# Performance work log

Measured on AMD Instinct MI355X. Metric: run time of the kernel, lower is better.

Reference implementation:

```python
import jax, jax.numpy as jnp
import numpy as np

DIM = 96
HEADS = 6
WS = 8                      # window_size
OWS = int(WS * 0.5) + WS    # overlap_win_size = 12
PAD = (OWS - WS) // 2       # 2
Dd = Hh = Ww = 24
B = 1
L = Dd * Hh * Ww
MLP_H = DIM * 2
TBL = (WS + OWS - 1) ** 3   # 6859 relative-position-bias entries


def setup_inputs() -> dict:
    key = jax.random.key(0)
    ks = jax.random.split(key, 8)
    def n(k, shape, s=0.02):
        return jax.random.normal(k, shape, jnp.float32) * s
    return {
        "x": jax.random.normal(ks[0], (B, L, DIM), jnp.float32),
        "ln1_w": jnp.ones((DIM,), jnp.float32),
        "ln1_b": jnp.zeros((DIM,), jnp.float32),
        "qkv_w": n(ks[1], (3 * DIM, DIM)),
        "qkv_b": jnp.zeros((3 * DIM,), jnp.float32),
        "rpb": n(ks[2], (TBL, HEADS)),
        "proj_w": n(ks[3], (DIM, DIM)),
        "proj_b": jnp.zeros((DIM,), jnp.float32),
        "ln2_w": jnp.ones((DIM,), jnp.float32),
        "ln2_b": jnp.zeros((DIM,), jnp.float32),
        "fc1_w": n(ks[4], (MLP_H, DIM)),
        "fc1_b": jnp.zeros((MLP_H,), jnp.float32),
        "fc2_w": n(ks[5], (DIM, MLP_H)),
        "fc2_b": jnp.zeros((DIM,), jnp.float32),
        "rpi": jax.random.randint(ks[6], (WS ** 3, OWS ** 3), 0, TBL),
        "D": Dd, "H": Hh, "W": Ww,
    }


def _ln(x, w, b):
    m = jnp.mean(x, -1, keepdims=True)
    v = jnp.var(x, -1, keepdims=True)
    return (x - m) / jnp.sqrt(v + 1e-5) * w + b


def _ocab3d(x, ln1_w, ln1_b, qkv_w, qkv_b, rpb, proj_w, proj_b,
            ln2_w, ln2_b, fc1_w, fc1_b, fc2_w, fc2_b, rpi, D, H, W):
    Bz, Lz, C = x.shape
    hd = C // HEADS
    scale = hd ** -0.5
    shortcut = x

    xn = _ln(x, ln1_w, ln1_b).reshape(Bz, D, H, W, C)
    qkv = xn @ qkv_w.T + qkv_b                   # [B,D,H,W,3C]
    q = qkv[..., :C]
    kv = qkv[..., C:]                            # cat(k, v) on channels, [B,D,H,W,2C]

    nD, nH, nW = D // WS, H // WS, W // WS
    nw = nD * nH * nW

    # non-overlapping query windows -> [B*nw, WS^3, C]
    qw = q.reshape(Bz, nD, WS, nH, WS, nW, WS, C)
    qw = qw.transpose(0, 1, 3, 5, 2, 4, 6, 7).reshape(Bz * nw, WS ** 3, C)

    # overlapping kv windows via pad + strided gather (mirrors F.pad + unfold)
    kvp = jnp.pad(kv, ((0, 0), (PAD, PAD), (PAD, PAD), (PAD, PAD), (0, 0)))
    idx_d = (jnp.arange(nD) * WS)[:, None] + jnp.arange(OWS)[None, :]
    idx_h = (jnp.arange(nH) * WS)[:, None] + jnp.arange(OWS)[None, :]
    idx_w = (jnp.arange(nW) * WS)[:, None] + jnp.arange(OWS)[None, :]
    kw = kvp[:, idx_d]                 # [B,nD,OWS,Hp,Wp,2C]
    kw = kw[:, :, :, idx_h]            # [B,nD,OWS,nH,OWS,Wp,2C]
    kw = kw[:, :, :, :, :, idx_w]      # [B,nD,OWS,nH,OWS,nW,OWS,2C]
    kw = kw.transpose(0, 1, 3, 5, 2, 4, 6, 7).reshape(Bz * nw, OWS ** 3, 2 * C)
    kk, vv = kw[..., :C], kw[..., C:]

    qh = qw.reshape(-1, WS ** 3, HEADS, hd).transpose(0, 2, 1, 3) * scale
    kh = kk.reshape(-1, OWS ** 3, HEADS, hd).transpose(0, 2, 1, 3)
    vh = vv.reshape(-1, OWS ** 3, HEADS, hd).transpose(0, 2, 1, 3)

    attn = jnp.einsum('bhqd,bhkd->bhqk', qh, kh)               # [B*nw,H,512,1728]
    bias = rpb[rpi.reshape(-1)].reshape(WS ** 3, OWS ** 3, HEADS).transpose(2, 0, 1)
    attn = jax.nn.softmax(attn + bias[None], axis=-1)
    out = jnp.einsum('bhqk,bhkd->bhqd', attn, vh)
    out = out.transpose(0, 2, 1, 3).reshape(Bz * nw, WS ** 3, C)

    # window reverse -> [B, L, C]
    out = out.reshape(Bz, nD, nH, nW, WS, WS, WS, C)
    out = out.transpose(0, 1, 4, 2, 5, 3, 6, 7).reshape(Bz, D * H * W, C)

    x2 = out @ proj_w.T + proj_b + shortcut
    h1 = jax.nn.gelu(_ln(x2, ln2_w, ln2_b) @ fc1_w.T + fc1_b, approximate=False)
    return x2 + (h1 @ fc2_w.T + fc2_b)


def reference(x, ln1_w, ln1_b, qkv_w, qkv_b, rpb, proj_w, proj_b,
              ln2_w, ln2_b, fc1_w, fc1_b, fc2_w, fc2_b, rpi, D, H, W):
    return _ocab3d(x, ln1_w, ln1_b, qkv_w, qkv_b, rpb, proj_w, proj_b,
                   ln2_w, ln2_b, fc1_w, fc1_b, fc2_w, fc2_b, rpi, D, H, W)
```

## Files before the change

### kernel.cpp

```cpp
#include <hip/hip_runtime.h>
#include <math.h>

#define DIMC   96
#define NHEADS 6
#define HD     16
#define WSZ    8
#define OWSZ   12
#define PADW   2
#define DD     24
#define LTOK   13824
#define NWIN   27
#define NKEY   1728
#define NROW   512
#define MLPH   192
#define PDIM   28
#define PD3    21952
#define TBL    6859
#define LSTR   82944
#define AOSTR  1327104

typedef __attribute__((ext_vector_type(4))) short bf16x4;
typedef __attribute__((ext_vector_type(8))) short bf16x8;
typedef __attribute__((ext_vector_type(4))) float f32x4;

__device__ __forceinline__ unsigned short bfround(float f) {
    unsigned u = __float_as_uint(f);
    return (unsigned short)((u + 0x7FFFu + ((u >> 16) & 1u)) >> 16);
}
__device__ __forceinline__ unsigned bfpack(float a, float b) {
    unsigned ua = __float_as_uint(a), ub = __float_as_uint(b);
    ua = (ua + 0x7FFFu + ((ua >> 16) & 1u)) >> 16;
    ub = (ub + 0x7FFFu + ((ub >> 16) & 1u)) >> 16;
    return ua | (ub << 16);
}
__device__ __forceinline__ uint4 pack8(const float* v) {
    uint4 u;
    u.x = bfpack(v[0], v[1]); u.y = bfpack(v[2], v[3]);
    u.z = bfpack(v[4], v[5]); u.w = bfpack(v[6], v[7]);
    return u;
}
__device__ __forceinline__ bf16x4 pack4(f32x4 p) {
    union { uint2 u; bf16x4 v; } r;
    r.u.x = __builtin_amdgcn_perm(__float_as_uint(p[1]), __float_as_uint(p[0]), 0x07060302u);
    r.u.y = __builtin_amdgcn_perm(__float_as_uint(p[3]), __float_as_uint(p[2]), 0x07060302u);
    return r.v;
}
__device__ __forceinline__ f32x4 mfma16(bf16x4 a, bf16x4 b, f32x4 c) {
#if __has_builtin(__builtin_amdgcn_mfma_f32_16x16x16bf16_1k)
    return __builtin_amdgcn_mfma_f32_16x16x16bf16_1k(a, b, c, 0, 0, 0);
#else
    bf16x8 a8 = {a[0], a[1], a[2], a[3], 0, 0, 0, 0};
    bf16x8 b8 = {b[0], b[1], b[2], b[3], 0, 0, 0, 0};
    return __builtin_amdgcn_mfma_f32_16x16x32_bf16(a8, b8, c, 0, 0, 0);
#endif
}

#define QKVB 1296
#define ZB   515
#define WPB  45
__global__ __launch_bounds__(256) void qkvz_kernel(
        const float* __restrict__ X, const float* __restrict__ W,
        const float* __restrict__ bias, const float* __restrict__ lnw,
        const float* __restrict__ lnb,
        const float* __restrict__ projw, const float* __restrict__ fc1w,
        const float* __restrict__ fc2w,
        unsigned short* __restrict__ q16, unsigned short* __restrict__ kvp2,
        uint4* __restrict__ wpack) {
    __shared__ uint4 Af4[2 * 3 * 4 * 16];
    __shared__ uint4 Bf4[6 * 3 * 4 * 16];
    int bx = blockIdx.x, tid = threadIdx.x;

    if (bx >= QKVB + ZB) {
        int u = (bx - QKVB - ZB) * 256 + tid;
        if (u < 5760) {
            int p = (u < 1152) ? u : (u < 3456 ? (u - 1152) % 1152 : (u - 3456) % 1152);
            int nn = p & 15, r = p >> 4, qg = r & 3, r2 = r >> 2;
            int kt = r2 % 3, ct = r2 / 3;
            int n = ct * 16 + nn, g = kt * 4 + qg;
            const float* src;
            if (u < 1152)      src = projw + n * 96 + g * 8;
            else if (u < 3456) { int nc = (u - 1152) / 1152; src = fc1w + (long)(nc * 96 + n) * 96 + g * 8; }
            else               { int kh = (u - 3456) / 1152; src = fc2w + (long)n * 192 + kh * 96 + g * 8; }
            const float4* s4 = (const float4*)src;
            float v[8];
            float4 t0 = s4[0], t1 = s4[1];
            v[0]=t0.x; v[1]=t0.y; v[2]=t0.z; v[3]=t0.w;
            v[4]=t1.x; v[5]=t1.y; v[6]=t1.z; v[7]=t1.w;
            wpack[u] = pack8(v);
        }
        return;
    }
    if (bx >= QKVB) {
        int t = (bx - QKVB) * 256 + tid;
        if (t < 21952 * 6) {
            int head = t / PD3, pos = t % PD3;
            int d = pos / 784, h = (pos / 28) % 28, w = pos % 28;
            if (d < 2 || d >= 26 || h < 2 || h >= 26 || w < 2 || w >= 26) {
                uint4* p = (uint4*)(kvp2 + ((long)head * PD3 + pos) * 32);
                uint4 z = make_uint4(0, 0, 0, 0);
                p[0] = z; p[1] = z; p[2] = z; p[3] = z;
            }
        }
        return;
    }

    int nc   = bx % 3;
    int row0 = (bx / 3) * 32;

    if (tid < 128) {
        int row = tid >> 2, part = tid & 3;
        int rt = row >> 4, mm = row & 15;
        float v[24];
        const float4* xp = (const float4*)(X + (long)(row0 + row) * 96 + part * 24);
        float s = 0.f, sq = 0.f;
        #pragma unroll
        for (int i = 0; i < 6; ++i) {
            float4 t = xp[i];
            v[i*4+0] = t.x; v[i*4+1] = t.y; v[i*4+2] = t.z; v[i*4+3] = t.w;
            s  += t.x + t.y + t.z + t.w;
            sq += t.x*t.x + t.y*t.y + t.z*t.z + t.w*t.w;
        }
        s  += __shfl_xor(s, 1);  s  += __shfl_xor(s, 2);
        sq += __shfl_xor(sq, 1); sq += __shfl_xor(sq, 2);
        float mean = s * (1.f / 96.f);
        float inv  = rsqrtf(sq * (1.f / 96.f) - mean * mean + 1e-5f);
        const float4* wp = (const float4*)(lnw + part * 24);
        const float4* bp = (const float4*)(lnb + part * 24);
        #pragma unroll
        for (int i = 0; i < 6; ++i) {
            float4 wv = wp[i], bv = bp[i];
            v[i*4+0] = (v[i*4+0] - mean) * inv * wv.x + bv.x;
            v[i*4+1] = (v[i*4+1] - mean) * inv * wv.y + bv.y;
            v[i*4+2] = (v[i*4+2] - mean) * inv * wv.z + bv.z;
            v[i*4+3] = (v[i*4+3] - mean) * inv * wv.w + bv.w;
        }
        #pragma unroll
        for (int gg = 0; gg < 3; ++gg) {
            int g = part * 3 + gg;
            int kt = g >> 2, qq = g & 3;
            Af4[((rt * 3 + kt) * 4 + qq) * 16 + mm] = pack8(v + gg * 8);
        }
    }
    for (int idx = tid; idx < 96 * 12; idx += 256) {
        int n = idx / 12;
        int g = idx % 12;
        const float4* wp = (const float4*)(W + (long)(nc * 96 + n) * 96 + g * 8);
        float v[8];
        float4 t0 = wp[0], t1 = wp[1];
        v[0]=t0.x; v[1]=t0.y; v[2]=t0.z; v[3]=t0.w;
        v[4]=t1.x; v[5]=t1.y; v[6]=t1.z; v[7]=t1.w;
        int ct = n >> 4, nn = n & 15, kt = g >> 2, qg = g & 3;
        Bf4[((ct * 3 + kt) * 4 + qg) * 16 + nn] = pack8(v);
    }
    __syncthreads();

    int wave = tid >> 6, lane = tid & 63;
    int qq = lane >> 4, mI = lane & 15;
    int rt = wave & 1, cg = wave >> 1;

    f32x4 acc[3];
    #pragma unroll
    for (int j = 0; j < 3; ++j) acc[j] = (f32x4){0.f, 0.f, 0.f, 0.f};
    #pragma unroll
    for (int kt = 0; kt < 3; ++kt) {
        bf16x8 a = *(const bf16x8*)&Af4[((rt * 3 + kt) * 4 + qq) * 16 + mI];
        #pragma unroll
        for (int j = 0; j < 3; ++j) {
            bf16x8 b = *(const bf16x8*)&Bf4[(((cg * 3 + j) * 3 + kt) * 4 + qq) * 16 + mI];
            acc[j] = __builtin_amdgcn_mfma_f32_16x16x32_bf16(a, b, acc[j], 0, 0, 0);
        }
    }

    float bv[3];
    #pragma unroll
    for (int j = 0; j < 3; ++j) bv[j] = bias[nc * 96 + (cg * 3 + j) * 16 + mI];
    #pragma unroll
    for (int r = 0; r < 4; ++r) {
        int row = row0 + rt * 16 + qq * 4 + r;
        if (nc == 0) {
            unsigned short* op = q16 + (long)row * 96;
            #pragma unroll
            for (int j = 0; j < 3; ++j)
                op[(cg * 3 + j) * 16 + mI] = bfround(0.25f * (acc[j][r] + bv[j]));
        } else {
            int d = row / 576, hh = (row / 24) % 24, w2 = row % 24;
            long pos = ((long)(d + 2) * 28 + (hh + 2)) * 28 + (w2 + 2);
            #pragma unroll
            for (int j = 0; j < 3; ++j) {
                int head = cg * 3 + j;
                kvp2[((long)head * PD3 + pos) * 32 +
                     (nc == 2 ? 16 : 0) + mI] = bfround(acc[j][r] + bv[j]);
            }
        }
    }
}

__global__ __launch_bounds__(256) void bias_kernel(
        const int* __restrict__ rpi, const float* __restrict__ rpb,
        float* __restrict__ biasP) {
    int bx = blockIdx.x;
    int head = bx / 216;
    int r2 = bx % 216;
    int kt = r2 >> 1, qh = r2 & 1;
    int k0 = kt * 16;
    int qi = qh * 256 + threadIdx.x;
    const int* rp = rpi + (long)qi * NKEY + k0;
    int idx[16];
    #pragma unroll
    for (int j = 0; j < 4; ++j) {
        int4 t = *(const int4*)(rp + j * 4);
        idx[j*4+0] = t.x; idx[j*4+1] = t.y; idx[j*4+2] = t.z; idx[j*4+3] = t.w;
    }
    #pragma unroll
    for (int quad = 0; quad < 4; ++quad) {
        float4 v;
        v.x = rpb[idx[quad*4+0] * NHEADS + head];
        v.y = rpb[idx[quad*4+1] * NHEADS + head];
        v.z = rpb[idx[quad*4+2] * NHEADS + head];
        v.w = rpb[idx[quad*4+3] * NHEADS + head];
        *(float4*)(biasP + ((((long)head*108 + kt)*4 + quad)*512 + qi)*4) = v;
    }
}

#define KSTR 20
#define VSTR 68
__global__ __launch_bounds__(256) void attn_kernel(
        const unsigned short* __restrict__ q, const unsigned short* __restrict__ kvp2,
        const float* __restrict__ biasP, float* __restrict__ ao,
        float* __restrict__ lbuf) {
    __shared__ unsigned short Ks[2][64 * KSTR];
    __shared__ unsigned short Vs[2][16 * VSTR];
    int bid = blockIdx.x;
    int w = bid / 48, rem = bid % 48;
    int head = rem >> 3;
    int quart = (rem >> 1) & 3, half = rem & 1;
    int wd8 = (w / 9) * 8, wh8 = ((w / 3) % 3) * 8, ww8 = (w % 3) * 8;
    int tid = threadIdx.x, wave = tid >> 6, lane = tid & 63;
    int quad = lane >> 4, m16 = lane & 15;
    int key = tid >> 2, part = tid & 3;
    int c0 = half ? 13 : 0;
    int cn = half ? 14 : 13;

    auto kvaddr = [&](int c) -> const uint4* {
        int jg = c * 64 + key;
        int i = jg / 144, jh = (jg / 12) % 12, jw = jg % 12;
        long sp = ((long)(wd8 + i) * PDIM + (wh8 + jh)) * PDIM + (ww8 + jw);
        return (const uint4*)(kvp2 + ((long)head * PD3 + sp) * 32 + part * 8);
    };
    auto writeLDS = [&](int b, uint4 v) {
        if (part < 2) {
            *(uint2*)(&Ks[b][key * KSTR + part * 8])     = make_uint2(v.x, v.y);
            *(uint2*)(&Ks[b][key * KSTR + part * 8 + 4]) = make_uint2(v.z, v.w);
        } else {
            int d0 = (part - 2) * 8;
            Vs[b][(d0+0)*VSTR + key] = (unsigned short)(v.x);
            Vs[b][(d0+1)*VSTR + key] = (unsigned short)(v.x >> 16);
            Vs[b][(d0+2)*VSTR + key] = (unsigned short)(v.y);
            Vs[b][(d0+3)*VSTR + key] = (unsigned short)(v.y >> 16);
            Vs[b][(d0+4)*VSTR + key] = (unsigned short)(v.z);
            Vs[b][(d0+5)*VSTR + key] = (unsigned short)(v.z >> 16);
            Vs[b][(d0+6)*VSTR + key] = (unsigned short)(v.w);
            Vs[b][(d0+7)*VSTR + key] = (unsigned short)(v.w >> 16);
        }
    };

    int grow[2]; bf16x4 qf[2];
    #pragma unroll
    for (int qt = 0; qt < 2; ++qt) {
        int ql = quart * 128 + wave * 32 + qt * 16 + m16;
        int ld = ql >> 6, lh = (ql >> 3) & 7, lw = ql & 7;
        grow[qt] = ((wd8 + ld) * 24 + (wh8 + lh)) * 24 + (ww8 + lw);
        qf[qt] = *(const bf16x4*)(q + (long)grow[qt] * 96 + head * 16 + quad * 4);
    }

    const float* bbase = biasP + (long)head * 884736 + quad * 2048
                         + ((quart * 128 + wave * 32 + m16) << 2);
    f32x4 bcur[2][4];
    #pragma unroll
    for (int qt = 0; qt < 2; ++qt)
        #pragma unroll
        for (int kt = 0; kt < 4; ++kt)
            bcur[qt][kt] = *(const f32x4*)(bbase + (long)(c0*4 + kt) * 8192 + qt * 64);

    writeLDS(0, *kvaddr(c0));

    f32x4 o[2];
    o[0] = (f32x4){0.f,0.f,0.f,0.f}; o[1] = (f32x4){0.f,0.f,0.f,0.f};
    float l[2] = {0.f, 0.f};
    uint4 stgn;

    #pragma unroll 1
    for (int cc = 0; cc < cn; ++cc) {
        int c = c0 + cc;
        if (cc + 1 < cn) stgn = *kvaddr(c + 1);
        __syncthreads();
        int b = cc & 1;

        bf16x4 kf[4];
        #pragma unroll
        for (int kt = 0; kt < 4; ++kt)
            kf[kt] = *(const bf16x4*)(&Ks[b][(kt * 16 + m16) * KSTR + quad * 4]);

        f32x4 S[2][4];
        #pragma unroll
        for (int qt = 0; qt < 2; ++qt)
            #pragma unroll
            for (int kt = 0; kt < 4; ++kt)
                S[qt][kt] = mfma16(kf[kt], qf[qt], bcur[qt][kt]);

        f32x4 bnxt[2][4];
        if (cc + 1 < cn) {
            const float* bp = bbase + (long)(c + 1) * 32768;
            #pragma unroll
            for (int qt = 0; qt < 2; ++qt)
                #pragma unroll
                for (int kt = 0; kt < 4; ++kt)
                    bnxt[qt][kt] = *(const f32x4*)(bp + kt * 8192 + qt * 64);
        }

        #pragma unroll
        for (int qt = 0; qt < 2; ++qt) {
            float ls = 0.f;
            #pragma unroll
            for (int kt = 0; kt < 4; ++kt)
                #pragma unroll
                for (int r = 0; r < 4; ++r) {
                    float p = __expf(S[qt][kt][r]);
                    S[qt][kt][r] = p; ls += p;
                }
            l[qt] += ls;
        }

        #pragma unroll
        for (int kt = 0; kt < 4; ++kt) {
            bf16x4 vf = *(const bf16x4*)(&Vs[b][m16 * VSTR + kt * 16 + quad * 4]);
            o[0] = mfma16(vf, pack4(S[0][kt]), o[0]);
            o[1] = mfma16(vf, pack4(S[1][kt]), o[1]);
        }

        if (cc + 1 < cn) writeLDS((cc + 1) & 1, stgn);
        #pragma unroll
        for (int qt = 0; qt < 2; ++qt)
            #pragma unroll
            for (int kt = 0; kt < 4; ++kt) bcur[qt][kt] = bnxt[qt][kt];
    }

    float* aout = ao + (long)half * AOSTR;
    float* lout = lbuf + (long)half * LSTR;
    #pragma unroll
    for (int qt = 0; qt < 2; ++qt) {
        float lq = l[qt];
        lq += __shfl_xor(lq, 16);
        lq += __shfl_xor(lq, 32);
        float4* op = (float4*)(aout + (long)grow[qt] * 96 + head * 16 + quad * 4);
        *op = make_float4(o[qt][0], o[qt][1], o[qt][2], o[qt][3]);
        if (quad == 0) lout[grow[qt] * 6 + head] = lq;
    }
}

__global__ __launch_bounds__(256) void mlp_kernel(
        const float* __restrict__ ao0, const float* __restrict__ ao1,
        const float* __restrict__ lbuf, const uint4* __restrict__ wpack,
        const float* __restrict__ projb, const float* __restrict__ x,
        const float* __restrict__ ln2w, const float* __restrict__ ln2b,
        const float* __restrict__ fc1b, const float* __restrict__ fc2b,
        float* __restrict__ out) {
    __shared__ uint4 Ws[5760];
    __shared__ uint4 Af4[2 * 3 * 4 * 16];
    __shared__ float x2s[32 * 96];
    __shared__ unsigned short h16[32 * 192];
    int tid = threadIdx.x;
    int row0 = blockIdx.x * 32;
    int wave = tid >> 6, lane = tid & 63;
    int qq = lane >> 4, mI = lane & 15;
    int rt = wave & 1, cg = wave >> 1;

    for (int idx = tid; idx < 5760; idx += 256) Ws[idx] = wpack[idx];

    if (tid < 128) {
        int row = tid >> 2, part = tid & 3;
        int rtA = row >> 4, mm = row & 15;
        int grow = row0 + row;
        const float4* a0 = (const float4*)(ao0 + (long)grow * 96 + part * 24);
        const float4* a1 = (const float4*)(ao1 + (long)grow * 96 + part * 24);
        int ha = (part * 3) >> 1, hb = ha + 1;
        float inva = 1.f / (lbuf[grow*6 + ha] + lbuf[LSTR + grow*6 + ha]);
        float invb = 1.f / (lbuf[grow*6 + hb] + lbuf[LSTR + grow*6 + hb]);
        float v[24];
        #pragma unroll
        for (int i = 0; i < 6; ++i) {
            float4 u0 = a0[i], u1 = a1[i];
            #pragma unroll
            for (int j = 0; j < 4; ++j) {
                int gc = part * 24 + i * 4 + j;
                float lv = ((gc >> 4) == ha) ? inva : invb;
                float s = (j==0?u0.x+u1.x : j==1?u0.y+u1.y : j==2?u0.z+u1.z : u0.w+u1.w);
                v[i*4+j] = s * lv;
            }
        }
        #pragma unroll
        for (int gg = 0; gg < 3; ++gg) {
            int g = part * 3 + gg;
            int kt = g >> 2, q4 = g & 3;
            Af4[((rtA * 3 + kt) * 4 + q4) * 16 + mm] = pack8(v + gg * 8);
        }
    }
    __syncthreads();

    {
        f32x4 acc[3];
        #pragma unroll
        for (int j = 0; j < 3; ++j) acc[j] = (f32x4){0.f,0.f,0.f,0.f};
        #pragma unroll
        for (int kt = 0; kt < 3; ++kt) {
            bf16x8 a = *(const bf16x8*)&Af4[((rt * 3 + kt) * 4 + qq) * 16 + mI];
            #pragma unroll
            for (int j = 0; j < 3; ++j) {
                bf16x8 b = *(const bf16x8*)&Ws[(((cg * 3 + j) * 3 + kt) * 4 + qq) * 16 + mI];
                acc[j] = __builtin_amdgcn_mfma_f32_16x16x32_bf16(a, b, acc[j], 0, 0, 0);
            }
        }
        float bv[3];
        #pragma unroll
        for (int j = 0; j < 3; ++j) bv[j] = projb[(cg * 3 + j) * 16 + mI];
        #pragma unroll
        for (int r = 0; r < 4; ++r) {
            int row = rt * 16 + qq * 4 + r;
            int grow = row0 + row;
            #pragma unroll
            for (int j = 0; j < 3; ++j) {
                int col = (cg * 3 + j) * 16 + mI;
                x2s[row * 96 + col] = acc[j][r] + bv[j] + x[(long)grow * 96 + col];
            }
        }
    }
    __syncthreads();

    if (tid < 128) {
        int row = tid >> 2, part = tid & 3;
        int rtA = row >> 4, mm = row & 15;
        float v[24];
        const float4* xp = (const float4*)(x2s + row * 96 + part * 24);
        float s = 0.f, sq = 0.f;
        #pragma unroll
        for (int i = 0; i < 6; ++i) {
            float4 t = xp[i];
            v[i*4+0] = t.x; v[i*4+1] = t.y; v[i*4+2] = t.z; v[i*4+3] = t.w;
            s  += t.x + t.y + t.z + t.w;
            sq += t.x*t.x + t.y*t.y + t.z*t.z + t.w*t.w;
        }
        s  += __shfl_xor(s, 1);  s  += __shfl_xor(s, 2);
        sq += __shfl_xor(sq, 1); sq += __shfl_xor(sq, 2);
        float mean = s * (1.f / 96.f);
        float inv  = rsqrtf(sq * (1.f / 96.f) - mean * mean + 1e-5f);
        const float4* wp = (const float4*)(ln2w + part * 24);
        const float4* bp = (const float4*)(ln2b + part * 24);
        #pragma unroll
        for (int i = 0; i < 6; ++i) {
            float4 wv = wp[i], bv = bp[i];
            v[i*4+0] = (v[i*4+0] - mean) * inv * wv.x + bv.x;
            v[i*4+1] = (v[i*4+1] - mean) * inv * wv.y + bv.y;
            v[i*4+2] = (v[i*4+2] - mean) * inv * wv.z + bv.z;
            v[i*4+3] = (v[i*4+3] - mean) * inv * wv.w + bv.w;
        }
        #pragma unroll
        for (int gg = 0; gg < 3; ++gg) {
            int g = part * 3 + gg;
            int kt = g >> 2, q4 = g & 3;
            Af4[((rtA * 3 + kt) * 4 + q4) * 16 + mm] = pack8(v + gg * 8);
        }
    }
    __syncthreads();

    #pragma unroll
    for (int nc = 0; nc < 2; ++nc) {
        f32x4 acc[3];
        #pragma unroll
        for (int j = 0; j < 3; ++j) acc[j] = (f32x4){0.f,0.f,0.f,0.f};
        #pragma unroll
        for (int kt = 0; kt < 3; ++kt) {
            bf16x8 a = *(const bf16x8*)&Af4[((rt * 3 + kt) * 4 + qq) * 16 + mI];
            #pragma unroll
            for (int j = 0; j < 3; ++j) {
                bf16x8 b = *(const bf16x8*)&Ws[1152 + nc * 1152 +
                               (((cg * 3 + j) * 3 + kt) * 4 + qq) * 16 + mI];
                acc[j] = __builtin_amdgcn_mfma_f32_16x16x32_bf16(a, b, acc[j], 0, 0, 0);
            }
        }
        float bv[3];
        #pragma unroll
        for (int j = 0; j < 3; ++j) bv[j] = fc1b[nc * 96 + (cg * 3 + j) * 16 + mI];
        #pragma unroll
        for (int r = 0; r < 4; ++r) {
            int row = rt * 16 + qq * 4 + r;
            #pragma unroll
            for (int j = 0; j < 3; ++j) {
                int col = nc * 96 + (cg * 3 + j) * 16 + mI;
                float v = acc[j][r] + bv[j];
                float g = 0.5f * v * (1.f + erff(v * 0.70710678f));
                int fi = (((row >> 4) * 6 + (col >> 5)) * 4 + ((col >> 3) & 3)) * 16 + (row & 15);
                h16[fi * 8 + (col & 7)] = bfround(g);
            }
        }
    }
    __syncthreads();

    f32x4 acc2[3];
    #pragma unroll
    for (int j = 0; j < 3; ++j) acc2[j] = (f32x4){0.f,0.f,0.f,0.f};
    #pragma unroll
    for (int kh = 0; kh < 2; ++kh) {
        #pragma unroll
        for (int kt = 0; kt < 3; ++kt) {
            int ktA = kh * 3 + kt;
            bf16x8 a = *(const bf16x8*)&h16[(((rt * 6 + ktA) * 4 + qq) * 16 + mI) * 8];
            #pragma unroll
            for (int j = 0; j < 3; ++j) {
                bf16x8 b = *(const bf16x8*)&Ws[3456 + kh * 1152 +
                               (((cg * 3 + j) * 3 + kt) * 4 + qq) * 16 + mI];
                acc2[j] = __builtin_amdgcn_mfma_f32_16x16x32_bf16(a, b, acc2[j], 0, 0, 0);
            }
        }
    }
    float bv[3];
    #pragma unroll
    for (int j = 0; j < 3; ++j) bv[j] = fc2b[(cg * 3 + j) * 16 + mI];
    #pragma unroll
    for (int r = 0; r < 4; ++r) {
        int row = rt * 16 + qq * 4 + r;
        int grow = row0 + row;
        #pragma unroll
        for (int j = 0; j < 3; ++j) {
            int col = (cg * 3 + j) * 16 + mI;
            out[(long)grow * 96 + col] = acc2[j][r] + bv[j] + x2s[row * 96 + col];
        }
    }
}

extern "C" void kernel_launch(void* const* d_in, const int* in_sizes, int n_in,
                              void* d_out, int out_size, void* d_ws, size_t ws_size,
                              hipStream_t stream) {
    const float* x     = (const float*)d_in[0];
    const float* ln1w  = (const float*)d_in[1];
    const float* ln1b  = (const float*)d_in[2];
    const float* qkvw  = (const float*)d_in[3];
    const float* qkvb  = (const float*)d_in[4];
    const float* rpb   = (const float*)d_in[5];
    const float* projw = (const float*)d_in[6];
    const float* projb = (const float*)d_in[7];
    const float* ln2w  = (const float*)d_in[8];
    const float* ln2b  = (const float*)d_in[9];
    const float* fc1w  = (const float*)d_in[10];
    const float* fc1b  = (const float*)d_in[11];
    const float* fc2w  = (const float*)d_in[12];
    const float* fc2b  = (const float*)d_in[13];
    const int*   rpi   = (const int*)d_in[14];
    float* outp = (float*)d_out;

    float* ws = (float*)d_ws;
    float*          aop    = ws;
    unsigned short* q16    = (unsigned short*)(ws + 2654208);
    unsigned short* kvp16  = (unsigned short*)(ws + 3317760);
    float*          biasPf = ws + 5425152;
    float*          lbuf   = ws + 10733568;
    uint4*          wpack  = (uint4*)(ws + 10899456);

    qkvz_kernel<<<QKVB + ZB + WPB, 256, 0, stream>>>(
        x, qkvw, qkvb, ln1w, ln1b, projw, fc1w, fc2w, q16, kvp16, wpack);
    bias_kernel<<<1296, 256, 0, stream>>>(rpi, rpb, biasPf);
    attn_kernel<<<NWIN * NHEADS * 4 * 2, 256, 0, stream>>>(q16, kvp16, biasPf, aop, lbuf);
    mlp_kernel<<<432, 256, 0, stream>>>(aop, aop + AOSTR, lbuf, wpack, projb, x,
                                        ln2w, ln2b, fc1b, fc2b, outp);
}
```

Before: 193.0 us.

## Fold log2e into q and bias, sum softmax rows via MFMA, enlarge MLP tiles

The scale factor log2(e) is folded into the q projection and the gathered bias table, so the attention loop can call the hardware exp2 directly instead of __expf. Row sums of P are now accumulated by an MFMA against a ones vector using the same bf16-packed probabilities, which replaces per-element scalar adds and cross-lane shuffles. The MLP kernel moves to 64-row tiles with 512 threads and a padded x2 shared-memory stride to cut bank conflicts and repeated weight staging. The denominator is now summed from bf16-rounded P, which stays consistent with the numerator but slightly changes precision. The larger MLP block also raises LDS use per block.

```diff
diff --git a/kernel.cpp b/kernel.cpp
--- a/kernel.cpp
+++ b/kernel.cpp
@@ -18,6 +18,7 @@
 #define TBL    6859
 #define LSTR   82944
 #define AOSTR  1327104
+#define LOG2E  1.4426950408889634f
 
 typedef __attribute__((ext_vector_type(4))) short bf16x4;
 typedef __attribute__((ext_vector_type(8))) short bf16x8;
@@ -52,6 +53,13 @@
     bf16x8 a8 = {a[0], a[1], a[2], a[3], 0, 0, 0, 0};
     bf16x8 b8 = {b[0], b[1], b[2], b[3], 0, 0, 0, 0};
     return __builtin_amdgcn_mfma_f32_16x16x32_bf16(a8, b8, c, 0, 0, 0);
+#endif
+}
+__device__ __forceinline__ float fexp2(float x) {
+#if __has_builtin(__builtin_amdgcn_exp2f)
+    return __builtin_amdgcn_exp2f(x);
+#else
+    return exp2f(x);
 #endif
 }
 
@@ -181,7 +189,7 @@
             unsigned short* op = q16 + (long)row * 96;
             #pragma unroll
             for (int j = 0; j < 3; ++j)
-                op[(cg * 3 + j) * 16 + mI] = bfround(0.25f * (acc[j][r] + bv[j]));
+                op[(cg * 3 + j) * 16 + mI] = bfround(0.25f * LOG2E * (acc[j][r] + bv[j]));
         } else {
             int d = row / 576, hh = (row / 24) % 24, w2 = row % 24;
             long pos = ((long)(d + 2) * 28 + (hh + 2)) * 28 + (w2 + 2);
@@ -214,10 +222,10 @@
     #pragma unroll
     for (int quad = 0; quad < 4; ++quad) {
         float4 v;
-        v.x = rpb[idx[quad*4+0] * NHEADS + head];
-        v.y = rpb[idx[quad*4+1] * NHEADS + head];
-        v.z = rpb[idx[quad*4+2] * NHEADS + head];
-        v.w = rpb[idx[quad*4+3] * NHEADS + head];
+        v.x = rpb[idx[quad*4+0] * NHEADS + head] * LOG2E;
+        v.y = rpb[idx[quad*4+1] * NHEADS + head] * LOG2E;
+        v.z = rpb[idx[quad*4+2] * NHEADS + head] * LOG2E;
+        v.w = rpb[idx[quad*4+3] * NHEADS + head] * LOG2E;
         *(float4*)(biasP + ((((long)head*108 + kt)*4 + quad)*512 + qi)*4) = v;
     }
 }
@@ -284,9 +292,10 @@
 
     writeLDS(0, *kvaddr(c0));
 
-    f32x4 o[2];
+    const bf16x4 onesf = {(short)0x3F80, (short)0x3F80, (short)0x3F80, (short)0x3F80};
+    f32x4 o[2], lacc[2];
     o[0] = (f32x4){0.f,0.f,0.f,0.f}; o[1] = (f32x4){0.f,0.f,0.f,0.f};
-    float l[2] = {0.f, 0.f};
+    lacc[0] = o[0]; lacc[1] = o[1];
     uint4 stgn;
 
     #pragma unroll 1
@@ -318,24 +327,23 @@
                     bnxt[qt][kt] = *(const f32x4*)(bp + kt * 8192 + qt * 64);
         }
 
-        #pragma unroll
-        for (int qt = 0; qt < 2; ++qt) {
-            float ls = 0.f;
-            #pragma unroll
-            for (int kt = 0; kt < 4; ++kt)
+        bf16x4 Pb[2][4];
+        #pragma unroll
+        for (int qt = 0; qt < 2; ++qt)
+            #pragma unroll
+            for (int kt = 0; kt < 4; ++kt) {
+                f32x4 p;
                 #pragma unroll
-                for (int r = 0; r < 4; ++r) {
-                    float p = __expf(S[qt][kt][r]);
-                    S[qt][kt][r] = p; ls += p;
-                }
-            l[qt] += ls;
-        }
+                for (int r = 0; r < 4; ++r) p[r] = fexp2(S[qt][kt][r]);
+                Pb[qt][kt] = pack4(p);
+                lacc[qt] = mfma16(onesf, Pb[qt][kt], lacc[qt]);
+            }
 
         #pragma unroll
         for (int kt = 0; kt < 4; ++kt) {
             bf16x4 vf = *(const bf16x4*)(&Vs[b][m16 * VSTR + kt * 16 + quad * 4]);
-            o[0] = mfma16(vf, pack4(S[0][kt]), o[0]);
-            o[1] = mfma16(vf, pack4(S[1][kt]), o[1]);
+            o[0] = mfma16(vf, Pb[0][kt], o[0]);
+            o[1] = mfma16(vf, Pb[1][kt], o[1]);
         }
 
         if (cc + 1 < cn) writeLDS((cc + 1) & 1, stgn);
@@ -349,16 +357,14 @@
     float* lout = lbuf + (long)half * LSTR;
     #pragma unroll
     for (int qt = 0; qt < 2; ++qt) {
-        float lq = l[qt];
-        lq += __shfl_xor(lq, 16);
-        lq += __shfl_xor(lq, 32);
         float4* op = (float4*)(aout + (long)grow[qt] * 96 + head * 16 + quad * 4);
         *op = make_float4(o[qt][0], o[qt][1], o[qt][2], o[qt][3]);
-        if (quad == 0) lout[grow[qt] * 6 + head] = lq;
-    }
-}
-
-__global__ __launch_bounds__(256) void mlp_kernel(
+        if (quad == 0) lout[grow[qt] * 6 + head] = lacc[qt][0];
+    }
+}
+
+#define X2S 100
+__global__ __launch_bounds__(512) void mlp_kernel(
         const float* __restrict__ ao0, const float* __restrict__ ao1,
         const float* __restrict__ lbuf, const uint4* __restrict__ wpack,
         const float* __restrict__ projb, const float* __restrict__ x,
@@ -366,18 +372,18 @@
         const float* __restrict__ fc1b, const float* __restrict__ fc2b,
         float* __restrict__ out) {
     __shared__ uint4 Ws[5760];
-    __shared__ uint4 Af4[2 * 3 * 4 * 16];
-    __shared__ float x2s[32 * 96];
-    __shared__ unsigned short h16[32 * 192];
+    __shared__ uint4 Af4[4 * 3 * 4 * 16];
+    __shared__ float x2s[64 * X2S];
+    __shared__ unsigned short h16[64 * 192];
     int tid = threadIdx.x;
-    int row0 = blockIdx.x * 32;
+    int row0 = blockIdx.x * 64;
     int wave = tid >> 6, lane = tid & 63;
     int qq = lane >> 4, mI = lane & 15;
-    int rt = wave & 1, cg = wave >> 1;
-
-    for (int idx = tid; idx < 5760; idx += 256) Ws[idx] = wpack[idx];
-
-    if (tid < 128) {
+    int rt = wave & 3, cg = wave >> 2;
+
+    for (int idx = tid; idx < 5760; idx += 512) Ws[idx] = wpack[idx];
+
+    if (tid < 256) {
         int row = tid >> 2, part = tid & 3;
         int rtA = row >> 4, mm = row & 15;
         int grow = row0 + row;
@@ -430,17 +436,17 @@
             #pragma unroll
             for (int j = 0; j < 3; ++j) {
                 int col = (cg * 3 + j) * 16 + mI;
-                x2s[row * 96 + col] = acc[j][r] + bv[j] + x[(long)grow * 96 + col];
+                x2s[row * X2S + col] = acc[j][r] + bv[j] + x[(long)grow * 96 + col];
             }
         }
     }
     __syncthreads();
 
-    if (tid < 128) {
+    if (tid < 256) {
         int row = tid >> 2, part = tid & 3;
         int rtA = row >> 4, mm = row & 15;
         float v[24];
-        const float4* xp = (const float4*)(x2s + row * 96 + part * 24);
+        const float4* xp = (const float4*)(x2s + row * X2S + part * 24);
         float s = 0.f, sq = 0.f;
         #pragma unroll
         for (int i = 0; i < 6; ++i) {
@@ -532,7 +538,7 @@
         #pragma unroll
         for (int j = 0; j < 3; ++j) {
             int col = (cg * 3 + j) * 16 + mI;
-            out[(long)grow * 96 + col] = acc2[j][r] + bv[j] + x2s[row * 96 + col];
+            out[(long)grow * 96 + col] = acc2[j][r] + bv[j] + x2s[row * X2S + col];
         }
     }
 }
@@ -569,6 +575,6 @@
         x, qkvw, qkvb, ln1w, ln1b, projw, fc1w, fc2w, q16, kvp16, wpack);
     bias_kernel<<<1296, 256, 0, stream>>>(rpi, rpb, biasPf);
     attn_kernel<<<NWIN * NHEADS * 4 * 2, 256, 0, stream>>>(q16, kvp16, biasPf, aop, lbuf);
-    mlp_kernel<<<432, 256, 0, stream>>>(aop, aop + AOSTR, lbuf, wpack, projb, x,
-                                        ln2w, ln2b, fc1b, fc2b, outp);
-}
+    mlp_kernel<<<LTOK / 64, 512, 0, stream>>>(aop, aop + AOSTR, lbuf, wpack, projb, x,
+                                              ln2w, ln2b, fc1b, fc2b, outp);
+}
```

After: 183.0 us. -5.2%, faster.
